# Kernel optimization log

Hardware: AMD Instinct MI355X
Metric: run time of the kernel (lower is better)

The kernel has to match this reference:

```python
import jax, jax.numpy as jnp
import numpy as np

NUM_HEADS = 16


def setup_inputs() -> dict:
    key = jax.random.key(0)
    k1, k2, k3, k4 = jax.random.split(key, 4)
    B, N, C = 4, 2048, 1024
    x = jax.random.normal(k1, (B, N, C), dtype=jnp.float32)
    g_info = jax.random.normal(k2, (2, 4, C), dtype=jnp.float32)
    qkv_w = jax.random.normal(k3, (3 * C, C), dtype=jnp.float32) * 0.02
    proj_w = jax.random.normal(k4, (C, C), dtype=jnp.float32) * 0.02
    proj_b = jnp.zeros((C,), dtype=jnp.float32)
    return {"x": x, "g_info": g_info, "qkv_w": qkv_w, "proj_w": proj_w, "proj_b": proj_b}


def reference(x, g_info, qkv_w, proj_w, proj_b):
    B, N, C = x.shape
    H = NUM_HEADS
    D = C // H
    scale = D ** -0.5
    # qkv projection (no bias): [B,N,3C] -> [B,N,3,H,D]
    qkv = (x @ qkv_w.T).reshape(B, N, 3, H, D)
    q, k, v = qkv[:, :, 0], qkv[:, :, 1], qkv[:, :, 2]  # each [B,N,H,D]
    # global-info fusion: g_info[0] -> (4,H,D); rows = q_g, k_g, v_g, t_g
    gl = g_info[0].reshape(4, H, D)
    q_g = gl[0][None, None]  # [1,1,H,D]
    k_g = gl[1][None, None]
    # NOTE: source computes min/max rescaled q_g/k_g but they are dead code;
    # the attention actually uses the unscaled additive fusion below.
    q_fused = q + q_g
    k_fused = k + k_g
    # memory_efficient_attention(q,k,v): softmax(q k^T / sqrt(D)) v
    attn = jnp.einsum("bqhd,bkhd->bhqk", q_fused, k_fused) * scale
    attn = jax.nn.softmax(attn, axis=-1)
    out = jnp.einsum("bhqk,bkhd->bqhd", attn, v).reshape(B, N, C)
    out = out @ proj_w.T + proj_b
    return (out, g_info[1:])
```

## Files before the change

kernel.cpp:

```cpp
#include <hip/hip_runtime.h>

typedef _Float16 h4 __attribute__((ext_vector_type(4)));
typedef _Float16 h8 __attribute__((ext_vector_type(8)));
typedef __fp16 fp16x2 __attribute__((ext_vector_type(2)));
typedef float f4 __attribute__((ext_vector_type(4)));
typedef float f16v __attribute__((ext_vector_type(16)));

#define MFMA16(a,b,c) __builtin_amdgcn_mfma_f32_16x16x32_f16(a, b, c, 0, 0, 0)
#define MFMA32(a,b,c) __builtin_amdgcn_mfma_f32_32x32x16_f16(a, b, c, 0, 0, 0)
#define EXP2(x) __builtin_amdgcn_exp2f(x)

__device__ __forceinline__ void gload_lds16(const _Float16* g, _Float16* l) {
    __builtin_amdgcn_global_load_lds((const __attribute__((address_space(1))) void*)g,
                                     (__attribute__((address_space(3))) void*)l, 16, 0, 0);
}

__device__ __forceinline__ void half_swap(float v, float& a, float& b) {
    unsigned x = __float_as_uint(v), y = x;
    asm("v_permlane32_swap_b32 %0, %1" : "+v"(x), "+v"(y));
    a = __uint_as_float(x); b = __uint_as_float(y);
}

__device__ __forceinline__ h8 ldfrag_sw(const _Float16* S, int R, int kk, int kq) {
    int b = kk * 4 + (kq >> 1);
    int o = (kq & 1) * 4;
    const _Float16* base = S + R * 64;
    h4 lo = *(const h4*)(base + ((b ^ (R & 7)) * 8) + o);
    h4 hi = *(const h4*)(base + (((b + 2) ^ (R & 7)) * 8) + o);
    return __builtin_shufflevector(lo, hi, 0, 1, 2, 3, 4, 5, 6, 7);
}

__device__ __forceinline__ void gemm_main(const _Float16* __restrict__ A, const _Float16* __restrict__ B,
                                          int K, int tM, int tN, int tid,
                                          _Float16* As, _Float16* Bs, f4 acc[4][4]) {
    int lane = tid & 63, w = tid >> 6;
    int wm = w >> 1, wn = w & 1;
    int ln = lane & 15, kq = lane >> 4;
    int r = tid >> 3;
    int sb = tid & 7;

    for (int k0 = 0; k0 < K; k0 += 64) {
#pragma unroll
        for (int it = 0; it < 4; ++it) {
            int row = r + it * 32;
            int srcb = sb ^ (row & 7);
            const _Float16* ga = A + (size_t)(tM * 128 + row) * K + k0 + srcb * 8;
            const _Float16* gb = B + (size_t)(tN * 128 + row) * K + k0 + srcb * 8;
            _Float16* la = As + ((tid & ~63) + it * 256) * 8;
            _Float16* lb = Bs + ((tid & ~63) + it * 256) * 8;
            gload_lds16(ga, la);
            gload_lds16(gb, lb);
        }
        __syncthreads();
#pragma unroll
        for (int kk = 0; kk < 2; ++kk) {
            h8 af[4], bf[4];
#pragma unroll
            for (int mi = 0; mi < 4; ++mi) af[mi] = ldfrag_sw(As, wm * 64 + mi * 16 + ln, kk, kq);
#pragma unroll
            for (int ni = 0; ni < 4; ++ni) bf[ni] = ldfrag_sw(Bs, wn * 64 + ni * 16 + ln, kk, kq);
#pragma unroll
            for (int mi = 0; mi < 4; ++mi)
#pragma unroll
                for (int ni = 0; ni < 4; ++ni) acc[mi][ni] = MFMA16(af[mi], bf[ni], acc[mi][ni]);
        }
        __syncthreads();
    }
}

__global__ __launch_bounds__(256) void k_cvt3(const float* __restrict__ x, const float* __restrict__ wq,
                                              const float* __restrict__ wp, _Float16* __restrict__ xh,
                                              _Float16* __restrict__ wqh, _Float16* __restrict__ wph) {
    const int NX = 1048576, NQ = 393216, NP = 131072;
    int stride = gridDim.x * blockDim.x;
    for (int s = blockIdx.x * blockDim.x + threadIdx.x; s < NX + NQ + NP; s += stride) {
        const float* src;
        _Float16* dst;
        int off;
        if (s < NX) { src = x; dst = xh; off = s; }
        else if (s < NX + NQ) { src = wq; dst = wqh; off = s - NX; }
        else { src = wp; dst = wph; off = s - NX - NQ; }
        float4 a = ((const float4*)src)[off * 2];
        float4 b = ((const float4*)src)[off * 2 + 1];
        h8 r = {(_Float16)a.x, (_Float16)a.y, (_Float16)a.z, (_Float16)a.w,
                (_Float16)b.x, (_Float16)b.y, (_Float16)b.z, (_Float16)b.w};
        ((h8*)dst)[off] = r;
    }
}

__global__ __launch_bounds__(256) void k_qkv(const _Float16* __restrict__ A, const _Float16* __restrict__ B,
                                             const float* __restrict__ g, _Float16* __restrict__ Qf,
                                             _Float16* __restrict__ Kf, _Float16* __restrict__ Vt) {
    __shared__ __align__(16) _Float16 As[128 * 64];
    __shared__ __align__(16) _Float16 Bs[128 * 64];
    int tid = threadIdx.x;
    int tN = blockIdx.x, tM = blockIdx.y;
    int lane = tid & 63, w = tid >> 6;
    int wm = w >> 1, wn = w & 1;
    int ln = lane & 15, kq = lane >> 4;

    f4 acc[4][4] = {};
    gemm_main(A, B, 1024, tM, tN, tid, As, Bs, acc);

#pragma unroll
    for (int mi = 0; mi < 4; ++mi) {
#pragma unroll
        for (int ni = 0; ni < 4; ++ni) {
#pragma unroll
            for (int r = 0; r < 4; ++r) {
                int gr = tM * 128 + wm * 64 + mi * 16 + kq * 4 + r;
                int gc = tN * 128 + wn * 64 + ni * 16 + ln;
                float val = acc[mi][ni][r];
                int which = gc >> 10;
                int c = gc & 1023, h = c >> 6, d = c & 63;
                int b = gr >> 11, n = gr & 2047;
                int bh = b * 16 + h;
                if (which == 0) {
                    val = (val + g[c]) * 0.18033688f;
                    Qf[((size_t)bh * 2048 + n) * 64 + d] = (_Float16)val;
                } else if (which == 1) {
                    val += g[1024 + c];
                    Kf[((size_t)bh * 2048 + n) * 64 + d] = (_Float16)val;
                } else {
                    Vt[((size_t)bh * 64 + d) * 2048 + n] = (_Float16)val;
                }
            }
        }
    }
}

__global__ __launch_bounds__(256) void k_attn(const _Float16* __restrict__ Qf, const _Float16* __restrict__ Kf,
                                              const _Float16* __restrict__ Vt, _Float16* __restrict__ Oa) {
    __shared__ __align__(16) _Float16 KV[2][2][64 * 64];
    int tid = threadIdx.x;
    int qt = blockIdx.x, bh = blockIdx.y;
    int lane = tid & 63, w = tid >> 6;
    int l31 = lane & 31, hi = lane >> 5;
    const _Float16* Qb = Qf + (size_t)bh * 2048 * 64;
    const _Float16* Kb = Kf + (size_t)bh * 2048 * 64;
    const _Float16* Vb = Vt + (size_t)bh * 64 * 2048;
    int qrow0 = qt * 128 + w * 32;

    int srow = tid >> 3, sblk = tid & 7;
    int sblk0 = (sblk ^ (srow & 7)) * 8;

#define STAGE(bufi, kvc)                                                                     \
    {                                                                                        \
        _Float16* lk = &KV[bufi][0][0] + ((tid & ~63)) * 8;                                  \
        _Float16* lv = &KV[bufi][1][0] + ((tid & ~63)) * 8;                                  \
        gload_lds16(Kb + (size_t)((kvc) + srow) * 64 + sblk0, lk);                           \
        gload_lds16(Kb + (size_t)((kvc) + srow + 32) * 64 + sblk0, lk + 2048);               \
        gload_lds16(Vb + (size_t)srow * 2048 + (kvc) + sblk0, lv);                           \
        gload_lds16(Vb + (size_t)(srow + 32) * 2048 + (kvc) + sblk0, lv + 2048);             \
    }

    h8 qfr[4];
#pragma unroll
    for (int dc = 0; dc < 4; ++dc)
        qfr[dc] = *(const h8*)(Qb + (size_t)(qrow0 + l31) * 64 + dc * 16 + hi * 8);

    f16v o0 = {}, o1 = {};
    float l_run = 0.f;

    STAGE(0, 0);
    __syncthreads();

    int cur = 0;
    for (int kvc = 0; kvc < 2048; kvc += 64) {
        if (kvc + 64 < 2048) STAGE(cur ^ 1, kvc + 64);

        const _Float16* Klc = &KV[cur][0][0];
        const _Float16* Vlc = &KV[cur][1][0];
        int sw = l31 & 7;

        f16v s0, s1;
#pragma unroll
        for (int r = 0; r < 16; ++r) { s0[r] = -4.f; s1[r] = -4.f; }
        __builtin_amdgcn_s_setprio(1);
#pragma unroll
        for (int dc = 0; dc < 4; ++dc) {
            int cb = dc * 2 + hi;
            h8 kf0 = *(const h8*)&Klc[l31 * 64 + ((cb ^ sw) * 8)];
            h8 kf1 = *(const h8*)&Klc[(32 + l31) * 64 + ((cb ^ sw) * 8)];
            s0 = MFMA32(kf0, qfr[dc], s0);
            s1 = MFMA32(kf1, qfr[dc], s1);
        }
        __builtin_amdgcn_s_setprio(0);

        float ps0[16], ps1[16];
#pragma unroll
        for (int r = 0; r < 16; ++r) ps0[r] = EXP2(s0[r]);
#pragma unroll
        for (int r = 0; r < 16; ++r) ps1[r] = EXP2(s1[r]);

        float t[16];
#pragma unroll
        for (int i = 0; i < 16; ++i) t[i] = ps0[i] + ps1[i];
#pragma unroll
        for (int i = 0; i < 8; ++i) t[i] += t[i + 8];
#pragma unroll
        for (int i = 0; i < 4; ++i) t[i] += t[i + 4];
        l_run += (t[0] + t[1]) + (t[2] + t[3]);

        unsigned W[16];
#pragma unroll
        for (int i = 0; i < 8; ++i) {
            union { fp16x2 h; unsigned u; } a, b;
            a.h = __builtin_amdgcn_cvt_pkrtz(ps0[2 * i], ps0[2 * i + 1]);
            b.h = __builtin_amdgcn_cvt_pkrtz(ps1[2 * i], ps1[2 * i + 1]);
            W[i] = a.u;
            W[8 + i] = b.u;
        }

        __builtin_amdgcn_s_setprio(1);
#pragma unroll
        for (int t2 = 0; t2 < 2; ++t2) {
#pragma unroll
            for (int kcl = 0; kcl < 2; ++kcl) {
                unsigned w0 = W[t2 * 8 + kcl * 4 + 0], w1 = W[t2 * 8 + kcl * 4 + 1];
                unsigned w2 = W[t2 * 8 + kcl * 4 + 2], w3 = W[t2 * 8 + kcl * 4 + 3];
                asm("v_permlane32_swap_b32 %0, %1" : "+v"(w0), "+v"(w2));
                asm("v_permlane32_swap_b32 %0, %1" : "+v"(w1), "+v"(w3));
                union { unsigned u[4]; h8 v; } pf;
                pf.u[0] = w0; pf.u[1] = w1; pf.u[2] = w2; pf.u[3] = w3;
                int cb = (t2 * 2 + kcl) * 2 + hi;
                h8 vf0 = *(const h8*)&Vlc[l31 * 64 + ((cb ^ sw) * 8)];
                h8 vf1 = *(const h8*)&Vlc[(32 + l31) * 64 + ((cb ^ sw) * 8)];
                o0 = MFMA32(pf.v, vf0, o0);
                o1 = MFMA32(pf.v, vf1, o1);
            }
        }
        __builtin_amdgcn_s_setprio(0);

        __syncthreads();
        cur ^= 1;
    }
#undef STAGE

    float la, lb;
    half_swap(l_run, la, lb);
    float inv = 1.f / (la + lb);
    int b = bh >> 4, h = bh & 15;
#pragma unroll
    for (int r = 0; r < 16; ++r) {
        int qloc = (r & 3) + 8 * (r >> 2) + 4 * hi;
        float iv = __shfl(inv, qloc, 64);
        size_t base = ((size_t)b * 2048 + qrow0 + qloc) * 1024 + h * 64;
        Oa[base + l31] = (_Float16)(o0[r] * iv);
        Oa[base + 32 + l31] = (_Float16)(o1[r] * iv);
    }
}

__global__ __launch_bounds__(256) void k_proj(const _Float16* __restrict__ A, const _Float16* __restrict__ B,
                                              const float* __restrict__ bias, float* __restrict__ out) {
    __shared__ __align__(16) _Float16 As[128 * 64];
    __shared__ __align__(16) _Float16 Bs[128 * 64];
    int tid = threadIdx.x;
    int tN = blockIdx.x, tM = blockIdx.y;
    int lane = tid & 63, w = tid >> 6;
    int wm = w >> 1, wn = w & 1;
    int ln = lane & 15, kq = lane >> 4;

    f4 acc[4][4] = {};
    gemm_main(A, B, 1024, tM, tN, tid, As, Bs, acc);

#pragma unroll
    for (int mi = 0; mi < 4; ++mi) {
#pragma unroll
        for (int ni = 0; ni < 4; ++ni) {
#pragma unroll
            for (int r = 0; r < 4; ++r) {
                int gr = tM * 128 + wm * 64 + mi * 16 + kq * 4 + r;
                int gc = tN * 128 + wn * 64 + ni * 16 + ln;
                out[(size_t)gr * 1024 + gc] = acc[mi][ni][r] + bias[gc];
            }
        }
    }
}

__global__ __launch_bounds__(256) void k_tail(const float* __restrict__ g, float* __restrict__ out) {
    int i = blockIdx.x * 256 + threadIdx.x;
    out[i] = g[4096 + i];
}

extern "C" void kernel_launch(void* const* d_in, const int* in_sizes, int n_in,
                              void* d_out, int out_size, void* d_ws, size_t ws_size,
                              hipStream_t stream) {
    const float* x = (const float*)d_in[0];
    const float* g = (const float*)d_in[1];
    const float* wq = (const float*)d_in[2];
    const float* wp = (const float*)d_in[3];
    const float* pb = (const float*)d_in[4];
    float* out = (float*)d_out;

    _Float16* xh = (_Float16*)d_ws;
    _Float16* wqh = xh + 8388608;
    _Float16* wph = wqh + 3145728;
    _Float16* Qf = wph + 1048576;
    _Float16* Kf = Qf + 8388608;
    _Float16* Vt = Kf + 8388608;
    _Float16* Oa = xh;

    k_cvt3<<<2048, 256, 0, stream>>>(x, wq, wp, xh, wqh, wph);
    k_qkv<<<dim3(24, 64), 256, 0, stream>>>(xh, wqh, g, Qf, Kf, Vt);
    k_attn<<<dim3(16, 64), 256, 0, stream>>>(Qf, Kf, Vt, Oa);
    k_proj<<<dim3(8, 64), 256, 0, stream>>>(Oa, wph, pb, out);
    k_tail<<<16, 256, 0, stream>>>(g, out + 8388608);
}
```

Measured before the change: 229.1 us.

## Enlarge GEMM block tiles to 256x128 with 8 waves and MFMA priority

The QKV and output-projection GEMMs now use 512-thread blocks, each computing a 256x128 tile instead of 128x128. The A tile in LDS doubles and the B tile is shared by twice as many waves, which cuts global/L2 traffic for B and halves the grid. The MFMA section is also wrapped in s_setprio so compute waves get scheduling priority. In exchange the grid is smaller (768 and 256 blocks), which may underfill the CUs, and each block uses more LDS.

```diff
diff --git a/kernel.cpp b/kernel.cpp
--- a/kernel.cpp
+++ b/kernel.cpp
@@ -33,8 +33,8 @@
 __device__ __forceinline__ void gemm_main(const _Float16* __restrict__ A, const _Float16* __restrict__ B,
                                           int K, int tM, int tN, int tid,
                                           _Float16* As, _Float16* Bs, f4 acc[4][4]) {
-    int lane = tid & 63, w = tid >> 6;
-    int wm = w >> 1, wn = w & 1;
+    int lane = tid & 63, wid = tid >> 6;
+    int wm4 = wid >> 1, wn2 = wid & 1;
     int ln = lane & 15, kq = lane >> 4;
     int r = tid >> 3;
     int sb = tid & 7;
@@ -42,28 +42,33 @@
     for (int k0 = 0; k0 < K; k0 += 64) {
 #pragma unroll
         for (int it = 0; it < 4; ++it) {
-            int row = r + it * 32;
+            int row = r + it * 64;
             int srcb = sb ^ (row & 7);
-            const _Float16* ga = A + (size_t)(tM * 128 + row) * K + k0 + srcb * 8;
-            const _Float16* gb = B + (size_t)(tN * 128 + row) * K + k0 + srcb * 8;
-            _Float16* la = As + ((tid & ~63) + it * 256) * 8;
-            _Float16* lb = Bs + ((tid & ~63) + it * 256) * 8;
-            gload_lds16(ga, la);
-            gload_lds16(gb, lb);
+            gload_lds16(A + (size_t)(tM * 256 + row) * K + k0 + srcb * 8,
+                        As + ((tid & ~63) + it * 512) * 8);
+        }
+#pragma unroll
+        for (int it = 0; it < 2; ++it) {
+            int row = r + it * 64;
+            int srcb = sb ^ (row & 7);
+            gload_lds16(B + (size_t)(tN * 128 + row) * K + k0 + srcb * 8,
+                        Bs + ((tid & ~63) + it * 512) * 8);
         }
         __syncthreads();
+        __builtin_amdgcn_s_setprio(1);
 #pragma unroll
         for (int kk = 0; kk < 2; ++kk) {
             h8 af[4], bf[4];
 #pragma unroll
-            for (int mi = 0; mi < 4; ++mi) af[mi] = ldfrag_sw(As, wm * 64 + mi * 16 + ln, kk, kq);
-#pragma unroll
-            for (int ni = 0; ni < 4; ++ni) bf[ni] = ldfrag_sw(Bs, wn * 64 + ni * 16 + ln, kk, kq);
+            for (int mi = 0; mi < 4; ++mi) af[mi] = ldfrag_sw(As, wm4 * 64 + mi * 16 + ln, kk, kq);
+#pragma unroll
+            for (int ni = 0; ni < 4; ++ni) bf[ni] = ldfrag_sw(Bs, wn2 * 64 + ni * 16 + ln, kk, kq);
 #pragma unroll
             for (int mi = 0; mi < 4; ++mi)
 #pragma unroll
                 for (int ni = 0; ni < 4; ++ni) acc[mi][ni] = MFMA16(af[mi], bf[ni], acc[mi][ni]);
         }
+        __builtin_amdgcn_s_setprio(0);
         __syncthreads();
     }
 }
@@ -88,15 +93,15 @@
     }
 }
 
-__global__ __launch_bounds__(256) void k_qkv(const _Float16* __restrict__ A, const _Float16* __restrict__ B,
+__global__ __launch_bounds__(512) void k_qkv(const _Float16* __restrict__ A, const _Float16* __restrict__ B,
                                              const float* __restrict__ g, _Float16* __restrict__ Qf,
                                              _Float16* __restrict__ Kf, _Float16* __restrict__ Vt) {
-    __shared__ __align__(16) _Float16 As[128 * 64];
+    __shared__ __align__(16) _Float16 As[256 * 64];
     __shared__ __align__(16) _Float16 Bs[128 * 64];
     int tid = threadIdx.x;
     int tN = blockIdx.x, tM = blockIdx.y;
-    int lane = tid & 63, w = tid >> 6;
-    int wm = w >> 1, wn = w & 1;
+    int lane = tid & 63, wid = tid >> 6;
+    int wm4 = wid >> 1, wn2 = wid & 1;
     int ln = lane & 15, kq = lane >> 4;
 
     f4 acc[4][4] = {};
@@ -108,8 +113,8 @@
         for (int ni = 0; ni < 4; ++ni) {
 #pragma unroll
             for (int r = 0; r < 4; ++r) {
-                int gr = tM * 128 + wm * 64 + mi * 16 + kq * 4 + r;
-                int gc = tN * 128 + wn * 64 + ni * 16 + ln;
+                int gr = tM * 256 + wm4 * 64 + mi * 16 + kq * 4 + r;
+                int gc = tN * 128 + wn2 * 64 + ni * 16 + ln;
                 float val = acc[mi][ni][r];
                 int which = gc >> 10;
                 int c = gc & 1023, h = c >> 6, d = c & 63;
@@ -251,14 +256,14 @@
     }
 }
 
-__global__ __launch_bounds__(256) void k_proj(const _Float16* __restrict__ A, const _Float16* __restrict__ B,
+__global__ __launch_bounds__(512) void k_proj(const _Float16* __restrict__ A, const _Float16* __restrict__ B,
                                               const float* __restrict__ bias, float* __restrict__ out) {
-    __shared__ __align__(16) _Float16 As[128 * 64];
+    __shared__ __align__(16) _Float16 As[256 * 64];
     __shared__ __align__(16) _Float16 Bs[128 * 64];
     int tid = threadIdx.x;
     int tN = blockIdx.x, tM = blockIdx.y;
-    int lane = tid & 63, w = tid >> 6;
-    int wm = w >> 1, wn = w & 1;
+    int lane = tid & 63, wid = tid >> 6;
+    int wm4 = wid >> 1, wn2 = wid & 1;
     int ln = lane & 15, kq = lane >> 4;
 
     f4 acc[4][4] = {};
@@ -270,8 +275,8 @@
         for (int ni = 0; ni < 4; ++ni) {
 #pragma unroll
             for (int r = 0; r < 4; ++r) {
-                int gr = tM * 128 + wm * 64 + mi * 16 + kq * 4 + r;
-                int gc = tN * 128 + wn * 64 + ni * 16 + ln;
+                int gr = tM * 256 + wm4 * 64 + mi * 16 + kq * 4 + r;
+                int gc = tN * 128 + wn2 * 64 + ni * 16 + ln;
                 out[(size_t)gr * 1024 + gc] = acc[mi][ni][r] + bias[gc];
             }
         }
@@ -302,8 +307,8 @@
     _Float16* Oa = xh;
 
     k_cvt3<<<2048, 256, 0, stream>>>(x, wq, wp, xh, wqh, wph);
-    k_qkv<<<dim3(24, 64), 256, 0, stream>>>(xh, wqh, g, Qf, Kf, Vt);
+    k_qkv<<<dim3(24, 32), 512, 0, stream>>>(xh, wqh, g, Qf, Kf, Vt);
     k_attn<<<dim3(16, 64), 256, 0, stream>>>(Qf, Kf, Vt, Oa);
-    k_proj<<<dim3(8, 64), 256, 0, stream>>>(Oa, wph, pb, out);
+    k_proj<<<dim3(8, 32), 512, 0, stream>>>(Oa, wph, pb, out);
     k_tail<<<16, 256, 0, stream>>>(g, out + 8388608);
 }
```

Result: slower. 264.8 us (+15.5%).
